# Kernel tuning notes

Measured on AMD Instinct MI355X. Metric: run time of the kernel, lower is better.

## Reference

```python
import jax, jax.numpy as jnp
import numpy as np

B, S, HID = 1, 2048, 2048
H, KH, D = 16, 8, 128          # query heads, kv heads, head_dim
GROUPS = H // KH                # num_key_value_groups = 2
EPS = 1e-6
SCALE = D ** -0.5
NEG = -1e9


def rmsnorm(x, w):
    # torch.nn.RMSNorm over last dim with learned weight
    return x * jax.lax.rsqrt(jnp.mean(x * x, axis=-1, keepdims=True) + EPS) * w


def rope(x, cos, sin):
    # x: [b, s, h, d]; cos/sin: [s, d//2]  (rotate-half style, matching apply_rotary_emb_single)
    half = x.shape[-1] // 2
    xr, xi = x[..., :half], x[..., half:]
    c = cos[None, :, None, :]
    s = sin[None, :, None, :]
    return jnp.concatenate([xr * c - xi * s, xr * s + xi * c], axis=-1)


def setup_inputs() -> dict:
    key = jax.random.key(0)
    ks = jax.random.split(key, 8)
    hidden_states = jax.random.normal(ks[0], (B, S, HID), jnp.float32)
    # real RoPE angle tables (theta=1e6, Qwen3-style), shape [S, D//2]
    inv_freq = 1.0 / (1e6 ** (np.arange(0, D, 2, dtype=np.float32) / D))
    ang = np.arange(S, dtype=np.float32)[:, None] * inv_freq[None, :]
    freqs_cos = jnp.asarray(np.cos(ang), jnp.float32)
    freqs_sin = jnp.asarray(np.sin(ang), jnp.float32)
    # additive causal mask [1, S, S]
    causal = jnp.tril(jnp.ones((S, S), jnp.bool_))
    atten_mask = jnp.where(causal, 0.0, NEG).astype(jnp.float32)[None]
    # learned params (no bias: attention_bias=False)
    Wq = jax.random.normal(ks[1], (H * D, HID), jnp.float32) * 0.02
    Wk = jax.random.normal(ks[2], (KH * D, HID), jnp.float32) * 0.02
    Wv = jax.random.normal(ks[3], (KH * D, HID), jnp.float32) * 0.02
    Wo = jax.random.normal(ks[4], (HID, H * D), jnp.float32) * 0.02
    q_norm_w = 1.0 + 0.01 * jax.random.normal(ks[5], (D,), jnp.float32)
    k_norm_w = 1.0 + 0.01 * jax.random.normal(ks[6], (D,), jnp.float32)
    return {"hidden_states": hidden_states, "freqs_cos": freqs_cos, "freqs_sin": freqs_sin,
            "atten_mask": atten_mask, "Wq": Wq, "Wk": Wk, "Wv": Wv, "Wo": Wo,
            "q_norm_w": q_norm_w, "k_norm_w": k_norm_w}


def reference(hidden_states, freqs_cos, freqs_sin, atten_mask, Wq, Wk, Wv, Wo, q_norm_w, k_norm_w):
    b, s, _ = hidden_states.shape
    q = (hidden_states @ Wq.T).reshape(b, s, H, D)
    k = (hidden_states @ Wk.T).reshape(b, s, KH, D)
    v = (hidden_states @ Wv.T).reshape(b, s, KH, D)
    q = rope(rmsnorm(q, q_norm_w), freqs_cos, freqs_sin)
    k = rope(rmsnorm(k, k_norm_w), freqs_cos, freqs_sin)
    # GQA: head i uses kv head i // GROUPS -> repeat kv heads in-order
    k_exp = jnp.repeat(k, GROUPS, axis=2)  # [b, s, H, d]
    v_exp = jnp.repeat(v, GROUPS, axis=2)
    scores = jnp.einsum('bshd,bthd->bhst', q, k_exp) * SCALE + atten_mask[:, None, :, :]
    attn = jax.nn.softmax(scores, axis=-1)
    y = jnp.einsum('bhst,bthd->bshd', attn, v_exp).reshape(b, s, H * D)
    y = y @ Wo.T
    # output_new_cache_only: last-position k (post-norm/RoPE) and raw v per kv head
    k_new = jnp.transpose(k[:, -1], (1, 0, 2))  # [KH, b, D]
    v_new = jnp.transpose(v[:, -1], (1, 0, 2))  # [KH, b, D]
    return y, k_new, v_new
```

## Files before the change

### kernel.cpp

```cpp
#include <hip/hip_runtime.h>
#include <hip/hip_bf16.h>
#include <math.h>

#define S_LEN 2048
#define HID 2048
#define NH 16
#define NKH 8
#define HD 128
#define QKV_N 4096
#define SCALE 0.08838834764831845f
#define EPS 1e-6f
#define LOG2E 1.4426950408889634f
#define QSCALE (SCALE * LOG2E)

typedef __hip_bfloat16 bf16;
typedef unsigned int u32;
typedef __bf16 bf16x8 __attribute__((ext_vector_type(8)));
typedef float f32x4 __attribute__((ext_vector_type(4)));

#define MFMA(a, b, c) __builtin_amdgcn_mfma_f32_16x16x32_bf16(a, b, c, 0, 0, 0)

static __device__ __forceinline__ bf16x8 ld_frag(const bf16* p) {
    return __builtin_bit_cast(bf16x8, *(const uint4*)p);
}

static __device__ __forceinline__ void gload_lds16(const void* g, void* l) {
    __builtin_amdgcn_global_load_lds(
        (const __attribute__((address_space(1))) u32*)g,
        (__attribute__((address_space(3))) u32*)l, 16, 0, 0);
}

__global__ __launch_bounds__(256) void cvt5(
    const float* __restrict__ s0, const float* __restrict__ s1,
    const float* __restrict__ s2, const float* __restrict__ s3,
    const float* __restrict__ s4,
    bf16* __restrict__ d0, bf16* __restrict__ d1, bf16* __restrict__ d2,
    bf16* __restrict__ d3, bf16* __restrict__ d4)
{
    int i = blockIdx.x * 256 + threadIdx.x;
    const float* s; bf16* d; int off;
    if (i < (1 << 20))                   { s = s0; d = d0; off = 0; }
    else if (i < (2 << 20))              { s = s1; d = d1; off = 1 << 20; }
    else if (i < (2 << 20) + (1 << 19))  { s = s2; d = d2; off = 2 << 20; }
    else if (i < (3 << 20))              { s = s3; d = d3; off = (2 << 20) + (1 << 19); }
    else                                 { s = s4; d = d4; off = 3 << 20; }
    int j = i - off;
    float4 v = ((const float4*)s)[j];
    union { ushort4 u; bf16 h[4]; } o;
    o.h[0] = __float2bfloat16(v.x);
    o.h[1] = __float2bfloat16(v.y);
    o.h[2] = __float2bfloat16(v.z);
    o.h[3] = __float2bfloat16(v.w);
    *(ushort4*)(d + 4 * (size_t)j) = o.u;
}

__global__ __launch_bounds__(256, 2) void gemm_qkv(
    const bf16* __restrict__ A, const bf16* __restrict__ B,
    bf16* __restrict__ qkvb, bf16* __restrict__ vT,
    const float* __restrict__ fcos, const float* __restrict__ fsin,
    const float* __restrict__ qw, const float* __restrict__ kw,
    float* __restrict__ knew, float* __restrict__ vnew)
{
    __shared__ bf16 As[2][128 * 64];
    __shared__ bf16 Bs[2][128 * 64];
    __shared__ float red[2][2][64];
    const int tid = threadIdx.x;
    const int n0 = blockIdx.x * 128, m0 = blockIdx.y * 128;
    const int w = tid >> 6, lane = tid & 63;
    const int l15 = lane & 15, quad = lane >> 4;
    const int wr = (w >> 1) * 64;
    const int wcg = (w & 1) * 32;

    f32x4 acc[4][4];
    #pragma unroll
    for (int i = 0; i < 4; ++i)
        #pragma unroll
        for (int j = 0; j < 4; ++j)
            acc[i][j] = f32x4{0.f, 0.f, 0.f, 0.f};

    const int srow8 = lane >> 3;
    const int sls = ((lane & 7) ^ srow8) * 8;

    auto stage = [&](int k0, int nb) {
        #pragma unroll
        for (int j = 0; j < 8; ++j) {
            int c = 8 * w + j;
            if (c < 16) {
                int row = c * 8 + srow8;
                gload_lds16(A + (size_t)(m0 + row) * HID + k0 + sls, &As[nb][c * 512]);
            } else {
                int row = (c - 16) * 8 + srow8;
                gload_lds16(B + (size_t)(n0 + row) * HID + k0 + sls, &Bs[nb][(c - 16) * 512]);
            }
        }
    };

    stage(0, 0);
    for (int kt = 0; kt < HID / 64; ++kt) {
        const int pp = kt & 1;
        __syncthreads();
        if (kt + 1 < HID / 64) stage((kt + 1) * 64, pp ^ 1);

        #pragma unroll
        for (int kc = 0; kc < 2; ++kc) {
            const int ph = ((kc * 4 + quad) ^ (l15 & 7)) * 8;
            bf16x8 av[4], bv[4];
            #pragma unroll
            for (int i = 0; i < 4; ++i)
                av[i] = ld_frag(&As[pp][(wr + i * 16 + l15) * 64 + ph]);
            #pragma unroll
            for (int j = 0; j < 4; ++j)
                bv[j] = ld_frag(&Bs[pp][(wcg + (j & 1) * 16 + (j >> 1) * 64 + l15) * 64 + ph]);
            #pragma unroll
            for (int i = 0; i < 4; ++i)
                #pragma unroll
                for (int j = 0; j < 4; ++j)
                    acc[i][j] = MFMA(av[i], bv[j], acc[i][j]);
        }
    }

    const int hblk = n0 >> 7;
    if (hblk < 24) {
        float ssq[4][4];
        #pragma unroll
        for (int i = 0; i < 4; ++i)
            #pragma unroll
            for (int rr = 0; rr < 4; ++rr) {
                float ss = 0.f;
                #pragma unroll
                for (int j = 0; j < 4; ++j) ss += acc[i][j][rr] * acc[i][j][rr];
                ss += __shfl_xor(ss, 1);
                ss += __shfl_xor(ss, 2);
                ss += __shfl_xor(ss, 4);
                ss += __shfl_xor(ss, 8);
                ssq[i][rr] = ss;
                if (l15 == 0)
                    red[w >> 1][w & 1][i * 16 + quad * 4 + rr] = ss;
            }
        __syncthreads();

        const float* wgt = (hblk < 16) ? qw : kw;
        float wv[4];
        #pragma unroll
        for (int j = 0; j < 4; ++j)
            wv[j] = wgt[wcg + (j & 1) * 16 + (j >> 1) * 64 + l15];
        const size_t cb = (hblk < 16) ? (size_t)hblk * HD
                                      : (size_t)HID + (size_t)(hblk - 16) * HD;

        #pragma unroll
        for (int i = 0; i < 4; ++i)
            #pragma unroll
            for (int rr = 0; rr < 4; ++rr) {
                int rloc = i * 16 + quad * 4 + rr;
                int srow = m0 + wr + rloc;
                float tot = ssq[i][rr] + red[w >> 1][(w & 1) ^ 1][rloc];
                float rrn = rsqrtf(tot * (1.0f / 128.0f) + EPS);
                float x[4], res[4];
                #pragma unroll
                for (int j = 0; j < 4; ++j) x[j] = acc[i][j][rr] * rrn * wv[j];
                #pragma unroll
                for (int j2 = 0; j2 < 2; ++j2) {
                    float c = fcos[srow * 64 + wcg + j2 * 16 + l15];
                    float s = fsin[srow * 64 + wcg + j2 * 16 + l15];
                    res[j2]     = x[j2] * c - x[j2 + 2] * s;
                    res[j2 + 2] = x[j2] * s + x[j2 + 2] * c;
                }
                if (hblk < 16) {
                    #pragma unroll
                    for (int j = 0; j < 4; ++j)
                        qkvb[(size_t)srow * QKV_N + cb + wcg + (j & 1) * 16 +
                             (j >> 1) * 64 + l15] = __float2bfloat16(res[j] * QSCALE);
                } else {
                    #pragma unroll
                    for (int j = 0; j < 4; ++j)
                        qkvb[(size_t)srow * QKV_N + cb + wcg + (j & 1) * 16 +
                             (j >> 1) * 64 + l15] = __float2bfloat16(res[j]);
                    if (srow == S_LEN - 1) {
                        #pragma unroll
                        for (int j = 0; j < 4; ++j)
                            knew[(hblk - 16) * HD + wcg + (j & 1) * 16 +
                                 (j >> 1) * 64 + l15] = res[j];
                    }
                }
            }
    } else {
        const int kh = hblk - 24;
        #pragma unroll
        for (int i = 0; i < 4; ++i) {
            int rowbase = m0 + wr + i * 16 + quad * 4;
            #pragma unroll
            for (int j = 0; j < 4; ++j) {
                int d = wcg + (j & 1) * 16 + (j >> 1) * 64 + l15;
                union { uint2 u; bf16 hh[4]; } pk;
                #pragma unroll
                for (int r = 0; r < 4; ++r)
                    pk.hh[r] = __float2bfloat16(acc[i][j][r]);
                *(uint2*)&vT[(size_t)(kh * HD + d) * S_LEN + rowbase] = pk.u;
                if (rowbase == S_LEN - 4)
                    vnew[kh * HD + d] = acc[i][j][3];
            }
        }
    }
}

__global__ __launch_bounds__(256, 2) void gemm_n64(
    const bf16* __restrict__ A, const bf16* __restrict__ B,
    float* __restrict__ C, int M, int N, int K)
{
    __shared__ bf16 As[2][128 * 64];
    __shared__ bf16 Bs[2][64 * 64];
    const int tid = threadIdx.x;
    const int n0 = blockIdx.x * 64, m0 = blockIdx.y * 128;
    const int w = tid >> 6, lane = tid & 63;
    const int l15 = lane & 15, quad = lane >> 4;

    f32x4 acc[2][4];
    #pragma unroll
    for (int i = 0; i < 2; ++i)
        #pragma unroll
        for (int j = 0; j < 4; ++j)
            acc[i][j] = f32x4{0.f, 0.f, 0.f, 0.f};

    const int srow8 = lane >> 3;
    const int sls = ((lane & 7) ^ srow8) * 8;

    auto stage = [&](int k0, int nb) {
        #pragma unroll
        for (int j = 0; j < 6; ++j) {
            int c = 6 * w + j;
            if (c < 16) {
                int row = c * 8 + srow8;
                gload_lds16(A + (size_t)(m0 + row) * K + k0 + sls, &As[nb][c * 512]);
            } else {
                int row = (c - 16) * 8 + srow8;
                gload_lds16(B + (size_t)(n0 + row) * K + k0 + sls, &Bs[nb][(c - 16) * 512]);
            }
        }
    };

    stage(0, 0);
    for (int kt = 0; kt < K / 64; ++kt) {
        const int pp = kt & 1;
        __syncthreads();
        if (kt + 1 < K / 64) stage((kt + 1) * 64, pp ^ 1);

        #pragma unroll
        for (int kc = 0; kc < 2; ++kc) {
            const int ph = ((kc * 4 + quad) ^ (l15 & 7)) * 8;
            bf16x8 av[2], bv[4];
            av[0] = ld_frag(&As[pp][(w * 32 + l15) * 64 + ph]);
            av[1] = ld_frag(&As[pp][(w * 32 + 16 + l15) * 64 + ph]);
            #pragma unroll
            for (int j = 0; j < 4; ++j)
                bv[j] = ld_frag(&Bs[pp][(j * 16 + l15) * 64 + ph]);
            #pragma unroll
            for (int i = 0; i < 2; ++i)
                #pragma unroll
                for (int j = 0; j < 4; ++j)
                    acc[i][j] = MFMA(av[i], bv[j], acc[i][j]);
        }
    }

    #pragma unroll
    for (int i = 0; i < 2; ++i)
        #pragma unroll
        for (int j = 0; j < 4; ++j)
            #pragma unroll
            for (int r = 0; r < 4; ++r)
                C[(size_t)(m0 + w * 32 + i * 16 + quad * 4 + r) * N +
                  n0 + j * 16 + l15] = acc[i][j][r];
}

__global__ __launch_bounds__(256, 2) void attn_mfma(
    const bf16* __restrict__ qkvb, const bf16* __restrict__ vT,
    bf16* __restrict__ outb)
{
    __shared__ bf16 Ks[2][64 * 128];
    __shared__ bf16 Vs[2][128 * 64];
    __shared__ bf16 Ps[4][16 * 72];
    __shared__ float lred[4][16];

    const int x = blockIdx.x;
    const int h = blockIdx.y, kvh = h >> 1;
    int a = (x & 1) ? (31 - (x >> 1)) : (x >> 1);
    const int qb = (h < 8) ? a : 31 - a;
    const int tid = threadIdx.x, w = tid >> 6, lane = tid & 63;
    const int l15 = lane & 15, quad = lane >> 4;
    const int qw0 = qb * 64 + w * 16;

    bf16x8 qf[4];
    #pragma unroll
    for (int dk = 0; dk < 4; ++dk)
        qf[dk] = ld_frag(qkvb + (size_t)(qw0 + l15) * QKV_N +
                         h * HD + dk * 32 + quad * 8);

    f32x4 o[8];
    #pragma unroll
    for (int dt = 0; dt < 8; ++dt) o[dt] = f32x4{0.f, 0.f, 0.f, 0.f};
    float l_st = 0.f;

    auto stage = [&](int t, int nb) {
        const int kt0 = t * 64;
        if (w < 2) {
            #pragma unroll
            for (int c = 0; c < 8; ++c) {
                int chunk = w * 8 + c;
                int row = 4 * chunk + (lane >> 4);
                int ls = (lane & 15) ^ (row & 15);
                gload_lds16(qkvb + (size_t)(kt0 + row) * QKV_N + HID +
                            kvh * HD + ls * 8,
                            &Ks[nb][chunk * 512]);
            }
        } else {
            #pragma unroll
            for (int c = 0; c < 8; ++c) {
                int chunk = (w - 2) * 8 + c;
                int row = 8 * chunk + (lane >> 3);
                int ls = (lane & 7) ^ ((lane >> 3) & 7);
                gload_lds16(vT + (size_t)(kvh * HD + row) * S_LEN + kt0 + ls * 8,
                            &Vs[nb][chunk * 512]);
            }
        }
    };

    stage(0, 0);
    for (int t = 0; t <= qb; ++t) {
        const int pp = t & 1;
        const int kt0 = t * 64;
        __syncthreads();
        if (t < qb) stage(t + 1, pp ^ 1);

        f32x4 sc[4];
        #pragma unroll
        for (int mt = 0; mt < 4; ++mt) sc[mt] = f32x4{0.f, 0.f, 0.f, 0.f};
        __builtin_amdgcn_s_setprio(1);
        #pragma unroll
        for (int dk = 0; dk < 4; ++dk)
            #pragma unroll
            for (int mt = 0; mt < 4; ++mt) {
                bf16x8 kf = ld_frag(&Ks[pp][(mt * 16 + l15) * 128 +
                                            (((dk * 4 + quad) ^ l15) & 15) * 8]);
                sc[mt] = MFMA(kf, qf[dk], sc[mt]);
            }
        __builtin_amdgcn_s_setprio(0);

        if (kt0 + 63 > qw0) {
            #pragma unroll
            for (int mt = 0; mt < 4; ++mt)
                #pragma unroll
                for (int r = 0; r < 4; ++r) {
                    int kg = kt0 + mt * 16 + quad * 4 + r;
                    if (kg > qw0 + l15) sc[mt][r] = -1e30f;
                }
        }

        #pragma unroll
        for (int mt = 0; mt < 4; ++mt) {
            union { uint2 u; bf16 hh[4]; } pk;
            #pragma unroll
            for (int r = 0; r < 4; ++r) {
                float p = exp2f(sc[mt][r]);
                pk.hh[r] = __float2bfloat16(p);
                l_st += p;
            }
            *(uint2*)&Ps[w][l15 * 72 + mt * 16 + quad * 4] = pk.u;
        }

        asm volatile("s_waitcnt lgkmcnt(0)" ::: "memory");
        __builtin_amdgcn_s_barrier();

        __builtin_amdgcn_s_setprio(1);
        #pragma unroll
        for (int kc = 0; kc < 2; ++kc) {
            bf16x8 pf[4];
            #pragma unroll
            for (int j = 0; j < 4; ++j)
                pf[j] = ld_frag(&Ps[j][l15 * 72 + kc * 32 + quad * 8]);
            #pragma unroll
            for (int dt = 0; dt < 2; ++dt) {
                bf16x8 vf = ld_frag(&Vs[pp][((w * 2 + dt) * 16 + l15) * 64 +
                                            (((kc * 4 + quad) ^ (l15 & 7)) * 8)]);
                #pragma unroll
                for (int j = 0; j < 4; ++j)
                    o[dt * 4 + j] = MFMA(vf, pf[j], o[dt * 4 + j]);
            }
        }
        __builtin_amdgcn_s_setprio(0);
    }

    l_st += __shfl_xor(l_st, 16, 64);
    l_st += __shfl_xor(l_st, 32, 64);
    if (lane < 16) lred[w][lane] = l_st;
    __syncthreads();
    #pragma unroll
    for (int j = 0; j < 4; ++j) {
        float inv = 1.0f / lred[j][l15];
        int qg = qb * 64 + j * 16 + l15;
        #pragma unroll
        for (int dt = 0; dt < 2; ++dt) {
            union { uint2 u; bf16 hh[4]; } pk;
            #pragma unroll
            for (int r = 0; r < 4; ++r)
                pk.hh[r] = __float2bfloat16(o[dt * 4 + j][r] * inv);
            *(uint2*)&outb[(size_t)qg * HID + h * HD + w * 32 + dt * 16 + quad * 4] = pk.u;
        }
    }
}

extern "C" void kernel_launch(void* const* d_in, const int* in_sizes, int n_in,
                              void* d_out, int out_size, void* d_ws, size_t ws_size,
                              hipStream_t stream) {
    const float* hidden = (const float*)d_in[0];
    const float* fcos   = (const float*)d_in[1];
    const float* fsin   = (const float*)d_in[2];
    const float* Wq = (const float*)d_in[4];
    const float* Wk = (const float*)d_in[5];
    const float* Wv = (const float*)d_in[6];
    const float* Wo = (const float*)d_in[7];
    const float* qw = (const float*)d_in[8];
    const float* kw = (const float*)d_in[9];
    float* out = (float*)d_out;

    bf16* qkvb  = (bf16*)d_ws;
    bf16* vT    = qkvb + (size_t)S_LEN * QKV_N;
    bf16* attnb = vT + (size_t)NKH * HD * S_LEN;
    bf16* wqkvb = attnb + (size_t)S_LEN * HID;
    bf16* hidb  = wqkvb + (size_t)QKV_N * HID;
    bf16* wob   = hidb + (size_t)S_LEN * HID;

    float* knew = out + (size_t)S_LEN * HID;
    float* vnew = knew + NKH * HD;

    cvt5<<<16384, 256, 0, stream>>>(
        hidden, Wq, Wk, Wv, Wo,
        hidb, wqkvb, wqkvb + (size_t)HID * HID,
        wqkvb + (size_t)(HID + NKH * HD) * HID, wob);

    gemm_qkv<<<dim3(QKV_N / 128, S_LEN / 128), 256, 0, stream>>>(
        hidb, wqkvb, qkvb, vT, fcos, fsin, qw, kw, knew, vnew);

    attn_mfma<<<dim3(32, NH), 256, 0, stream>>>(qkvb, vT, attnb);

    gemm_n64<<<dim3(HID / 64, S_LEN / 128), 256, 0, stream>>>(
        attnb, wob, out, S_LEN, HID, HID);
}
```

Measured before the change: 239.7 us.

## Restructure QKV GEMM to two-wave blocks with triple-buffered K=32 pipeline

The QKV projection GEMM now runs 128-thread blocks. Each of the two waves owns a full 128x64 output slice with 8x4 accumulators, and one wave loads A while the other loads B. The K loop uses 32-wide tiles in a three-stage LDS ring with explicit vmcnt waits, so two tiles stay in flight and each step needs one barrier. The aim is more MFMA work per wave and better latency hiding, at the cost of higher register pressure and fewer waves per CU. Separately, the s_setprio hints are removed from the attention kernel.

```diff
diff --git a/kernel.cpp b/kernel.cpp
--- a/kernel.cpp
+++ b/kernel.cpp
@@ -54,76 +54,75 @@
     *(ushort4*)(d + 4 * (size_t)j) = o.u;
 }
 
-__global__ __launch_bounds__(256, 2) void gemm_qkv(
+__global__ __launch_bounds__(128, 2) void gemm_qkv(
     const bf16* __restrict__ A, const bf16* __restrict__ B,
     bf16* __restrict__ qkvb, bf16* __restrict__ vT,
     const float* __restrict__ fcos, const float* __restrict__ fsin,
     const float* __restrict__ qw, const float* __restrict__ kw,
     float* __restrict__ knew, float* __restrict__ vnew)
 {
-    __shared__ bf16 As[2][128 * 64];
-    __shared__ bf16 Bs[2][128 * 64];
-    __shared__ float red[2][2][64];
+    __shared__ bf16 As[3][128 * 32];
+    __shared__ bf16 Bs[3][128 * 32];
+    __shared__ float red[2][128];
     const int tid = threadIdx.x;
     const int n0 = blockIdx.x * 128, m0 = blockIdx.y * 128;
     const int w = tid >> 6, lane = tid & 63;
     const int l15 = lane & 15, quad = lane >> 4;
-    const int wr = (w >> 1) * 64;
-    const int wcg = (w & 1) * 32;
-
-    f32x4 acc[4][4];
-    #pragma unroll
-    for (int i = 0; i < 4; ++i)
+    const int wcg = w * 32;
+
+    f32x4 acc[8][4];
+    #pragma unroll
+    for (int i = 0; i < 8; ++i)
         #pragma unroll
         for (int j = 0; j < 4; ++j)
             acc[i][j] = f32x4{0.f, 0.f, 0.f, 0.f};
 
-    const int srow8 = lane >> 3;
-    const int sls = ((lane & 7) ^ srow8) * 8;
+    const int srow = lane >> 2;
+    const int sls = ((lane & 3) ^ (srow & 3)) * 8;
 
     auto stage = [&](int k0, int nb) {
         #pragma unroll
-        for (int j = 0; j < 8; ++j) {
-            int c = 8 * w + j;
-            if (c < 16) {
-                int row = c * 8 + srow8;
-                gload_lds16(A + (size_t)(m0 + row) * HID + k0 + sls, &As[nb][c * 512]);
-            } else {
-                int row = (c - 16) * 8 + srow8;
-                gload_lds16(B + (size_t)(n0 + row) * HID + k0 + sls, &Bs[nb][(c - 16) * 512]);
-            }
+        for (int c = 0; c < 8; ++c) {
+            if (w == 0)
+                gload_lds16(A + (size_t)(m0 + c * 16 + srow) * HID + k0 + sls,
+                            &As[nb][c * 512]);
+            else
+                gload_lds16(B + (size_t)(n0 + c * 16 + srow) * HID + k0 + sls,
+                            &Bs[nb][c * 512]);
         }
     };
 
     stage(0, 0);
-    for (int kt = 0; kt < HID / 64; ++kt) {
-        const int pp = kt & 1;
-        __syncthreads();
-        if (kt + 1 < HID / 64) stage((kt + 1) * 64, pp ^ 1);
-
-        #pragma unroll
-        for (int kc = 0; kc < 2; ++kc) {
-            const int ph = ((kc * 4 + quad) ^ (l15 & 7)) * 8;
-            bf16x8 av[4], bv[4];
-            #pragma unroll
-            for (int i = 0; i < 4; ++i)
-                av[i] = ld_frag(&As[pp][(wr + i * 16 + l15) * 64 + ph]);
+    stage(32, 1);
+    #pragma unroll 1
+    for (int kt = 0; kt < 64; ++kt) {
+        asm volatile("s_waitcnt lgkmcnt(0)" ::: "memory");
+        if (kt < 63) asm volatile("s_waitcnt vmcnt(8)" ::: "memory");
+        else         asm volatile("s_waitcnt vmcnt(0)" ::: "memory");
+        __builtin_amdgcn_s_barrier();
+        const int cb = kt % 3;
+        if (kt + 2 < 64) stage((kt + 2) * 32, (kt + 2) % 3);
+
+        const int ph = (quad ^ (l15 & 3)) * 8;
+        bf16x8 av[8], bv[4];
+        #pragma unroll
+        for (int i = 0; i < 8; ++i)
+            av[i] = ld_frag(&As[cb][(i * 16 + l15) * 32 + ph]);
+        #pragma unroll
+        for (int j = 0; j < 4; ++j)
+            bv[j] = ld_frag(&Bs[cb][(wcg + (j & 1) * 16 + (j >> 1) * 64 + l15) * 32 + ph]);
+        #pragma unroll
+        for (int i = 0; i < 8; ++i)
             #pragma unroll
             for (int j = 0; j < 4; ++j)
-                bv[j] = ld_frag(&Bs[pp][(wcg + (j & 1) * 16 + (j >> 1) * 64 + l15) * 64 + ph]);
-            #pragma unroll
-            for (int i = 0; i < 4; ++i)
-                #pragma unroll
-                for (int j = 0; j < 4; ++j)
-                    acc[i][j] = MFMA(av[i], bv[j], acc[i][j]);
-        }
+                acc[i][j] = MFMA(av[i], bv[j], acc[i][j]);
     }
 
     const int hblk = n0 >> 7;
     if (hblk < 24) {
-        float ssq[4][4];
-        #pragma unroll
-        for (int i = 0; i < 4; ++i)
+        float ssq[8][4];
+        #pragma unroll
+        for (int i = 0; i < 8; ++i)
             #pragma unroll
             for (int rr = 0; rr < 4; ++rr) {
                 float ss = 0.f;
@@ -135,7 +134,7 @@
                 ss += __shfl_xor(ss, 8);
                 ssq[i][rr] = ss;
                 if (l15 == 0)
-                    red[w >> 1][w & 1][i * 16 + quad * 4 + rr] = ss;
+                    red[w][i * 16 + quad * 4 + rr] = ss;
             }
         __syncthreads();
 
@@ -144,38 +143,38 @@
         #pragma unroll
         for (int j = 0; j < 4; ++j)
             wv[j] = wgt[wcg + (j & 1) * 16 + (j >> 1) * 64 + l15];
-        const size_t cb = (hblk < 16) ? (size_t)hblk * HD
-                                      : (size_t)HID + (size_t)(hblk - 16) * HD;
-
-        #pragma unroll
-        for (int i = 0; i < 4; ++i)
+        const size_t cb2 = (hblk < 16) ? (size_t)hblk * HD
+                                       : (size_t)HID + (size_t)(hblk - 16) * HD;
+
+        #pragma unroll
+        for (int i = 0; i < 8; ++i)
             #pragma unroll
             for (int rr = 0; rr < 4; ++rr) {
                 int rloc = i * 16 + quad * 4 + rr;
-                int srow = m0 + wr + rloc;
-                float tot = ssq[i][rr] + red[w >> 1][(w & 1) ^ 1][rloc];
+                int srow_g = m0 + rloc;
+                float tot = ssq[i][rr] + red[w ^ 1][rloc];
                 float rrn = rsqrtf(tot * (1.0f / 128.0f) + EPS);
                 float x[4], res[4];
                 #pragma unroll
                 for (int j = 0; j < 4; ++j) x[j] = acc[i][j][rr] * rrn * wv[j];
                 #pragma unroll
                 for (int j2 = 0; j2 < 2; ++j2) {
-                    float c = fcos[srow * 64 + wcg + j2 * 16 + l15];
-                    float s = fsin[srow * 64 + wcg + j2 * 16 + l15];
+                    float c = fcos[srow_g * 64 + wcg + j2 * 16 + l15];
+                    float s = fsin[srow_g * 64 + wcg + j2 * 16 + l15];
                     res[j2]     = x[j2] * c - x[j2 + 2] * s;
                     res[j2 + 2] = x[j2] * s + x[j2 + 2] * c;
                 }
                 if (hblk < 16) {
                     #pragma unroll
                     for (int j = 0; j < 4; ++j)
-                        qkvb[(size_t)srow * QKV_N + cb + wcg + (j & 1) * 16 +
+                        qkvb[(size_t)srow_g * QKV_N + cb2 + wcg + (j & 1) * 16 +
                              (j >> 1) * 64 + l15] = __float2bfloat16(res[j] * QSCALE);
                 } else {
                     #pragma unroll
                     for (int j = 0; j < 4; ++j)
-                        qkvb[(size_t)srow * QKV_N + cb + wcg + (j & 1) * 16 +
+                        qkvb[(size_t)srow_g * QKV_N + cb2 + wcg + (j & 1) * 16 +
                              (j >> 1) * 64 + l15] = __float2bfloat16(res[j]);
-                    if (srow == S_LEN - 1) {
+                    if (srow_g == S_LEN - 1) {
                         #pragma unroll
                         for (int j = 0; j < 4; ++j)
                             knew[(hblk - 16) * HD + wcg + (j & 1) * 16 +
@@ -186,8 +185,8 @@
     } else {
         const int kh = hblk - 24;
         #pragma unroll
-        for (int i = 0; i < 4; ++i) {
-            int rowbase = m0 + wr + i * 16 + quad * 4;
+        for (int i = 0; i < 8; ++i) {
+            int rowbase = m0 + i * 16 + quad * 4;
             #pragma unroll
             for (int j = 0; j < 4; ++j) {
                 int d = wcg + (j & 1) * 16 + (j >> 1) * 64 + l15;
@@ -333,7 +332,6 @@
         f32x4 sc[4];
         #pragma unroll
         for (int mt = 0; mt < 4; ++mt) sc[mt] = f32x4{0.f, 0.f, 0.f, 0.f};
-        __builtin_amdgcn_s_setprio(1);
         #pragma unroll
         for (int dk = 0; dk < 4; ++dk)
             #pragma unroll
@@ -342,7 +340,6 @@
                                             (((dk * 4 + quad) ^ l15) & 15) * 8]);
                 sc[mt] = MFMA(kf, qf[dk], sc[mt]);
             }
-        __builtin_amdgcn_s_setprio(0);
 
         if (kt0 + 63 > qw0) {
             #pragma unroll
@@ -369,7 +366,6 @@
         asm volatile("s_waitcnt lgkmcnt(0)" ::: "memory");
         __builtin_amdgcn_s_barrier();
 
-        __builtin_amdgcn_s_setprio(1);
         #pragma unroll
         for (int kc = 0; kc < 2; ++kc) {
             bf16x8 pf[4];
@@ -385,7 +381,6 @@
                     o[dt * 4 + j] = MFMA(vf, pf[j], o[dt * 4 + j]);
             }
         }
-        __builtin_amdgcn_s_setprio(0);
     }
 
     l_st += __shfl_xor(l_st, 16, 64);
@@ -436,7 +431,7 @@
         hidb, wqkvb, wqkvb + (size_t)HID * HID,
         wqkvb + (size_t)(HID + NKH * HD) * HID, wob);
 
-    gemm_qkv<<<dim3(QKV_N / 128, S_LEN / 128), 256, 0, stream>>>(
+    gemm_qkv<<<dim3(QKV_N / 128, S_LEN / 128), 128, 0, stream>>>(
         hidb, wqkvb, qkvb, vT, fcos, fsin, qw, kw, knew, vnew);
 
     attn_mfma<<<dim3(32, NH), 256, 0, stream>>>(qkvb, vT, attnb);
```

Result: slower. 259.8 us (+8.4%).
